# Kernel optimization log

Measured on AMD Instinct MI355X. Metric: run time of the kernel, lower is better.

The kernel has to match this reference:

```python
import jax, jax.numpy as jnp
import numpy as np

N_VERTICES = 1_000_000
N_EDGES = 16_000_000


def setup_inputs() -> dict:
    key = jax.random.key(0)
    k1, k2, k3 = jax.random.split(key, 3)
    vertex_attr = jax.random.normal(k1, (N_VERTICES, 2), dtype=jnp.float32)
    edgeij_pair = jax.random.randint(k2, (2, N_EDGES), 0, N_VERTICES, dtype=jnp.int64)
    edge_attr = jax.random.normal(k3, (N_EDGES, 2), dtype=jnp.float32)
    g = jnp.zeros((1, 1), dtype=jnp.float32)
    batch = jnp.zeros((N_VERTICES,), dtype=jnp.int64)
    return {"vertex_attr": vertex_attr, "edgeij_pair": edgeij_pair,
            "edge_attr": edge_attr, "g": g, "batch": batch}


def reference(vertex_attr, edgeij_pair, edge_attr, g, batch):
    # c_ij: second edge feature column, [E, 1]
    c_ij = edge_attr[:, 1:2]
    b_i = vertex_attr[:, 0:1]  # [N, 1]
    x_i = vertex_attr[:, 1:2]  # [N, 1]
    n_vertices = x_i.shape[0]
    # edge-to-vertex aggregation: sum c_ij into receiving vertex i (row 0)
    cbar_i = jax.ops.segment_sum(c_ij, edgeij_pair[0], num_segments=n_vertices)
    r_i = b_i - cbar_i
    return jnp.concatenate([b_i, x_i, r_i], axis=1)  # [N, 3]
```

## Files before the change

kernel.cpp:

```cpp
#include <hip/hip_runtime.h>


#define BSHIFT 11
#define BSIZE (1 << BSHIFT)
#define NBUCK_PAD 512
#define TILE 8192
#define TPB 1024
#define PGRID 512
#define NREP 8

#define BARL() do { \
    asm volatile("s_waitcnt lgkmcnt(0)" ::: "memory"); \
    __builtin_amdgcn_s_barrier(); } while (0)

__global__ __launch_bounds__(TPB, 8)
void vu_partition(const int* __restrict__ src,
                  const float* __restrict__ eattr,
                  unsigned long long* __restrict__ pairs,
                  unsigned int* __restrict__ alloc,
                  int ne, int nbuck, int cap_r) {
    __shared__ unsigned long long sorted[TILE];
    __shared__ unsigned int hist[NBUCK_PAD];
    __shared__ unsigned int base_l[NBUCK_PAD];
    __shared__ unsigned int cursor[NBUCK_PAD];
    __shared__ unsigned int gbase[NBUCK_PAD];
    __shared__ unsigned int wsum[8];

    const int t = threadIdx.x;
    const int rep = blockIdx.x & (NREP - 1);
    const int nt_tiles = (ne + TILE - 1) / TILE;

    int   s0, s1, s2, s3, s4, s5, s6, s7;
    float c0, c1, c2, c3, c4, c5, c6, c7;

    int tk = blockIdx.x;

    if (tk < nt_tiles) {
        int tile0 = tk * TILE;
        if (tile0 + TILE <= ne) {
            const int* sp = src + tile0 + t;
            const float* cp = eattr + 2 * (tile0 + t) + 1;
            s0 = sp[0 * 1024]; s1 = sp[1 * 1024];
            s2 = sp[2 * 1024]; s3 = sp[3 * 1024];
            s4 = sp[4 * 1024]; s5 = sp[5 * 1024];
            s6 = sp[6 * 1024]; s7 = sp[7 * 1024];
            c0 = cp[0 * 2048]; c1 = cp[1 * 2048];
            c2 = cp[2 * 2048]; c3 = cp[3 * 2048];
            c4 = cp[4 * 2048]; c5 = cp[5 * 2048];
            c6 = cp[6 * 2048]; c7 = cp[7 * 2048];
        }
    }
    if (t < NBUCK_PAD) hist[t] = 0u;
    BARL();

    for (; tk < nt_tiles; tk += PGRID) {
        int tile0 = tk * TILE;
        int lim = ne - tile0; if (lim > TILE) lim = TILE;
        bool full = (lim == TILE);

        int nk = tk + PGRID;
        bool pv = (nk < nt_tiles) && (nk * TILE + TILE <= ne);
        int   p0s, p1s, p2s, p3s, p4s, p5s, p6s, p7s;
        float p0c, p1c, p2c, p3c, p4c, p5c, p6c, p7c;
        if (pv) {
            int ptile0 = nk * TILE;
            const int* sp = src + ptile0 + t;
            const float* cp = eattr + 2 * (ptile0 + t) + 1;
            p0s = sp[0 * 1024]; p1s = sp[1 * 1024];
            p2s = sp[2 * 1024]; p3s = sp[3 * 1024];
            p4s = sp[4 * 1024]; p5s = sp[5 * 1024];
            p6s = sp[6 * 1024]; p7s = sp[7 * 1024];
            p0c = cp[0 * 2048]; p1c = cp[1 * 2048];
            p2c = cp[2 * 2048]; p3c = cp[3 * 2048];
            p4c = cp[4 * 2048]; p5c = cp[5 * 2048];
            p6c = cp[6 * 2048]; p7c = cp[7 * 2048];
        }

        if (full) {
            atomicAdd(&hist[((unsigned)s0) >> BSHIFT], 1u);
            atomicAdd(&hist[((unsigned)s1) >> BSHIFT], 1u);
            atomicAdd(&hist[((unsigned)s2) >> BSHIFT], 1u);
            atomicAdd(&hist[((unsigned)s3) >> BSHIFT], 1u);
            atomicAdd(&hist[((unsigned)s4) >> BSHIFT], 1u);
            atomicAdd(&hist[((unsigned)s5) >> BSHIFT], 1u);
            atomicAdd(&hist[((unsigned)s6) >> BSHIFT], 1u);
            atomicAdd(&hist[((unsigned)s7) >> BSHIFT], 1u);
        } else {
            for (int i = t; i < lim; i += TPB)
                atomicAdd(&hist[((unsigned)src[tile0 + i]) >> BSHIFT], 1u);
        }
        BARL();

        unsigned int mycnt = (t < NBUCK_PAD) ? hist[t] : 0u;
        if (t < NBUCK_PAD) hist[t] = 0u;
        unsigned int gb = 0u;
        if (t < nbuck && mycnt)
            gb = atomicAdd(&alloc[rep * NBUCK_PAD + t], mycnt);

        unsigned int x = mycnt;
        #pragma unroll
        for (int off = 1; off < 64; off <<= 1) {
            unsigned int v = __shfl_up(x, off, 64);
            if ((t & 63) >= off) x += v;
        }
        if (t < NBUCK_PAD && (t & 63) == 63) wsum[t >> 6] = x;
        BARL();

        unsigned int wx = 0u;
        int wid = t >> 6;
        #pragma unroll
        for (int k = 0; k < 7; ++k) {
            unsigned int w = wsum[k];
            if (k < wid) wx += w;
        }
        if (t < NBUCK_PAD) {
            unsigned int excl = x + wx - mycnt;
            base_l[t] = excl;
            cursor[t] = excl;
            gbase[t] = gb;
        }
        BARL();

#define VU_SCAT(sv, cv) do { \
        unsigned int q_ = ((unsigned)(sv)) >> BSHIFT; \
        unsigned int pos_ = atomicAdd(&cursor[q_], 1u); \
        sorted[pos_] = ((unsigned long long)__float_as_uint(cv) << 32) \
                       | (unsigned)(sv); } while (0)
        if (full) {
            VU_SCAT(s0, c0); VU_SCAT(s1, c1);
            VU_SCAT(s2, c2); VU_SCAT(s3, c3);
            VU_SCAT(s4, c4); VU_SCAT(s5, c5);
            VU_SCAT(s6, c6); VU_SCAT(s7, c7);
        } else {
            for (int i = t; i < lim; i += TPB) {
                int e = tile0 + i;
                int s = src[e];
                float2 ec = ((const float2*)eattr)[e];
                VU_SCAT(s, ec.y);
            }
        }
#undef VU_SCAT
        BARL();

        for (int i = t; i < lim; i += TPB) {
            unsigned long long p = sorted[i];
            unsigned int q = ((unsigned int)p) >> BSHIFT;
            unsigned int seg = (q << 3) + (unsigned int)rep;
            unsigned int dst = seg * (unsigned int)cap_r + gbase[q]
                             + ((unsigned int)i - base_l[q]);
            unsigned int hi = seg * (unsigned int)cap_r + (unsigned int)cap_r - 1u;
            if (dst > hi) dst = hi;
            pairs[dst] = p;
        }

        s0 = p0s; s1 = p1s; s2 = p2s; s3 = p3s;
        s4 = p4s; s5 = p5s; s6 = p6s; s7 = p7s;
        c0 = p0c; c1 = p1c; c2 = p2c; c3 = p3c;
        c4 = p4c; c5 = p5c; c6 = p6c; c7 = p7c;
    }
}

__global__ __launch_bounds__(1024)
void vu_aggregate(const unsigned long long* __restrict__ pairs,
                  const unsigned int* __restrict__ alloc,
                  const float* __restrict__ vattr,
                  float* __restrict__ out,
                  int nv, int cap_r) {
    __shared__ float acc[BSIZE];
    __shared__ float obuf[BSIZE * 3];
    int q = blockIdx.x;
    int t = threadIdx.x;
    acc[t] = 0.0f;
    acc[t + 1024] = 0.0f;

    int v0 = q << BSHIFT;
    int iv0 = v0 + t, iv1 = v0 + t + 1024;
    float2 va0 = make_float2(0.f, 0.f), va1 = make_float2(0.f, 0.f);
    if (iv0 < nv) va0 = ((const float2*)vattr)[iv0];
    if (iv1 < nv) va1 = ((const float2*)vattr)[iv1];

    unsigned int cnts[NREP];
    #pragma unroll
    for (int r = 0; r < NREP; ++r) {
        unsigned int c = alloc[r * NBUCK_PAD + q];
        cnts[r] = (c > (unsigned int)cap_r) ? (unsigned int)cap_r : c;
    }
    __syncthreads();

#define VU_ACC(v64) do { \
        atomicAdd(&acc[((unsigned int)(v64)) & (BSIZE - 1)], \
                  __uint_as_float((unsigned int)((v64) >> 32))); } while (0)

    #pragma unroll
    for (int r = 0; r < NREP; ++r) {
        unsigned int cnt = cnts[r];
        const unsigned long long* p =
            pairs + (size_t)(q * NREP + r) * (size_t)cap_r;
        const ulonglong2* p2 = (const ulonglong2*)p;
        unsigned int n2 = cnt >> 1;
        for (unsigned int i = t; i < n2; i += 1024u) {
            ulonglong2 v = p2[i];
            VU_ACC(v.x); VU_ACC(v.y);
        }
        if (t == 0 && (cnt & 1u)) {
            unsigned long long v = p[cnt - 1];
            VU_ACC(v);
        }
    }
#undef VU_ACC
    __syncthreads();

    if (iv0 < nv) {
        obuf[3 * t + 0] = va0.x;
        obuf[3 * t + 1] = va0.y;
        obuf[3 * t + 2] = va0.x - acc[t];
    }
    {
        int i2 = t + 1024;
        if (iv1 < nv) {
            obuf[3 * i2 + 0] = va1.x;
            obuf[3 * i2 + 1] = va1.y;
            obuf[3 * i2 + 2] = va1.x - acc[i2];
        }
    }
    __syncthreads();

    long fbase = (long)q * (BSIZE * 3);
    int nfl = 3 * nv - (int)fbase;
    if (nfl > BSIZE * 3) nfl = BSIZE * 3;
    if (nfl > 0) {
        float4* o4 = (float4*)(out + fbase);
        const float4* s4 = (const float4*)obuf;
        int n4 = nfl >> 2;
        for (int j = t; j < n4; j += 1024) o4[j] = s4[j];
        for (int j = (n4 << 2) + t; j < nfl; j += 1024) out[fbase + j] = obuf[j];
    }
}

__global__ void vu_init_kernel(const float* __restrict__ vattr,
                               float* __restrict__ out, int n) {
    int i = blockIdx.x * blockDim.x + threadIdx.x;
    if (i < n) {
        float2 v = ((const float2*)vattr)[i];
        out[3 * i + 0] = v.x;
        out[3 * i + 1] = v.y;
        out[3 * i + 2] = v.x;
    }
}

__global__ void vu_scatter_kernel(const int* __restrict__ src,
                                  const float* __restrict__ eattr,
                                  float* __restrict__ out, int ne) {
    int t = blockIdx.x * blockDim.x + threadIdx.x;
    int e0 = t * 4;
    if (e0 + 3 < ne) {
        int4 idx = ((const int4*)src)[t];
        float4 a = ((const float4*)eattr)[2 * t + 0];
        float4 b = ((const float4*)eattr)[2 * t + 1];
        atomicAdd(&out[3 * idx.x + 2], -a.y);
        atomicAdd(&out[3 * idx.y + 2], -a.w);
        atomicAdd(&out[3 * idx.z + 2], -b.y);
        atomicAdd(&out[3 * idx.w + 2], -b.w);
    } else {
        for (int e = e0; e < ne; ++e)
            atomicAdd(&out[3 * src[e] + 2], -eattr[2 * e + 1]);
    }
}

extern "C" void kernel_launch(void* const* d_in, const int* in_sizes, int n_in,
                              void* d_out, int out_size, void* d_ws, size_t ws_size,
                              hipStream_t stream) {
    const float* vattr = (const float*)d_in[0];
    const int* edges = (const int*)d_in[1];
    const float* eattr = (const float*)d_in[2];
    float* out = (float*)d_out;

    int nv = in_sizes[0] / 2;
    int ne = in_sizes[2] / 2;

    int nbuck = (nv + BSIZE - 1) >> BSHIFT;
    int mean_r = ne / nbuck / NREP;
    int cap_r = mean_r + mean_r / 8;
    cap_r = (cap_r + 15) & ~15;

    size_t alloc_bytes = (size_t)NREP * NBUCK_PAD * 4;
    size_t pair_bytes = (size_t)nbuck * NREP * (size_t)cap_r * 8ull;
    size_t need = alloc_bytes + pair_bytes;

    if (ws_size >= need && nbuck <= NBUCK_PAD) {
        unsigned int* alloc = (unsigned int*)d_ws;
        unsigned long long* pairs = (unsigned long long*)((char*)d_ws + alloc_bytes);
        (void)hipMemsetAsync(alloc, 0, alloc_bytes, stream);

        int nt_tiles = (ne + TILE - 1) / TILE;
        int grid = PGRID; if (grid > nt_tiles) grid = nt_tiles;
        vu_partition<<<grid, TPB, 0, stream>>>(edges, eattr, pairs, alloc,
                                               ne, nbuck, cap_r);
        vu_aggregate<<<nbuck, 1024, 0, stream>>>(pairs, alloc, vattr, out,
                                                 nv, cap_r);
    } else {
        int threads = 256;
        int blocks = (nv + threads - 1) / threads;
        vu_init_kernel<<<blocks, threads, 0, stream>>>(vattr, out, nv);
        int nt = (ne + 3) / 4;
        blocks = (nt + threads - 1) / threads;
        vu_scatter_kernel<<<blocks, threads, 0, stream>>>(edges, eattr, out, ne);
    }
}
```

Baseline: 373.3 us.

## Replace persistent prefetching partition loop with one-tile-per-block launch and vector loads

The partition kernel no longer runs as a persistent grid that loops over tiles with software prefetch of the next tile. It now launches one 512-thread block per 4096-edge tile, loading each thread's 8 consecutive sources and edge attributes with int4/float4 vector loads. The hist array is reused to hold the global bases, dropping the separate gbase array and cutting shared memory so more blocks can be resident. This trades the register-level prefetch overlap for occupancy-driven latency hiding, at the cost of more blocks and more global atomics on alloc. Each block's output runs are also shorter.

```diff
diff --git a/kernel.cpp b/kernel.cpp
--- a/kernel.cpp
+++ b/kernel.cpp
@@ -4,9 +4,8 @@
 #define BSHIFT 11
 #define BSIZE (1 << BSHIFT)
 #define NBUCK_PAD 512
-#define TILE 8192
-#define TPB 1024
-#define PGRID 512
+#define TILE 4096
+#define TPB 512
 #define NREP 8
 
 #define BARL() do { \
@@ -23,140 +22,98 @@
     __shared__ unsigned int hist[NBUCK_PAD];
     __shared__ unsigned int base_l[NBUCK_PAD];
     __shared__ unsigned int cursor[NBUCK_PAD];
-    __shared__ unsigned int gbase[NBUCK_PAD];
     __shared__ unsigned int wsum[8];
 
     const int t = threadIdx.x;
     const int rep = blockIdx.x & (NREP - 1);
-    const int nt_tiles = (ne + TILE - 1) / TILE;
-
-    int   s0, s1, s2, s3, s4, s5, s6, s7;
+    const int tile0 = blockIdx.x * TILE;
+    int lim = ne - tile0; if (lim > TILE) lim = TILE;
+    const bool full = (lim == TILE);
+
+    hist[t] = 0u;
+    BARL();
+
+    int4 sa, sb;
     float c0, c1, c2, c3, c4, c5, c6, c7;
-
-    int tk = blockIdx.x;
-
-    if (tk < nt_tiles) {
-        int tile0 = tk * TILE;
-        if (tile0 + TILE <= ne) {
-            const int* sp = src + tile0 + t;
-            const float* cp = eattr + 2 * (tile0 + t) + 1;
-            s0 = sp[0 * 1024]; s1 = sp[1 * 1024];
-            s2 = sp[2 * 1024]; s3 = sp[3 * 1024];
-            s4 = sp[4 * 1024]; s5 = sp[5 * 1024];
-            s6 = sp[6 * 1024]; s7 = sp[7 * 1024];
-            c0 = cp[0 * 2048]; c1 = cp[1 * 2048];
-            c2 = cp[2 * 2048]; c3 = cp[3 * 2048];
-            c4 = cp[4 * 2048]; c5 = cp[5 * 2048];
-            c6 = cp[6 * 2048]; c7 = cp[7 * 2048];
-        }
-    }
-    if (t < NBUCK_PAD) hist[t] = 0u;
-    BARL();
-
-    for (; tk < nt_tiles; tk += PGRID) {
-        int tile0 = tk * TILE;
-        int lim = ne - tile0; if (lim > TILE) lim = TILE;
-        bool full = (lim == TILE);
-
-        int nk = tk + PGRID;
-        bool pv = (nk < nt_tiles) && (nk * TILE + TILE <= ne);
-        int   p0s, p1s, p2s, p3s, p4s, p5s, p6s, p7s;
-        float p0c, p1c, p2c, p3c, p4c, p5c, p6c, p7c;
-        if (pv) {
-            int ptile0 = nk * TILE;
-            const int* sp = src + ptile0 + t;
-            const float* cp = eattr + 2 * (ptile0 + t) + 1;
-            p0s = sp[0 * 1024]; p1s = sp[1 * 1024];
-            p2s = sp[2 * 1024]; p3s = sp[3 * 1024];
-            p4s = sp[4 * 1024]; p5s = sp[5 * 1024];
-            p6s = sp[6 * 1024]; p7s = sp[7 * 1024];
-            p0c = cp[0 * 2048]; p1c = cp[1 * 2048];
-            p2c = cp[2 * 2048]; p3c = cp[3 * 2048];
-            p4c = cp[4 * 2048]; p5c = cp[5 * 2048];
-            p6c = cp[6 * 2048]; p7c = cp[7 * 2048];
-        }
-
-        if (full) {
-            atomicAdd(&hist[((unsigned)s0) >> BSHIFT], 1u);
-            atomicAdd(&hist[((unsigned)s1) >> BSHIFT], 1u);
-            atomicAdd(&hist[((unsigned)s2) >> BSHIFT], 1u);
-            atomicAdd(&hist[((unsigned)s3) >> BSHIFT], 1u);
-            atomicAdd(&hist[((unsigned)s4) >> BSHIFT], 1u);
-            atomicAdd(&hist[((unsigned)s5) >> BSHIFT], 1u);
-            atomicAdd(&hist[((unsigned)s6) >> BSHIFT], 1u);
-            atomicAdd(&hist[((unsigned)s7) >> BSHIFT], 1u);
-        } else {
-            for (int i = t; i < lim; i += TPB)
-                atomicAdd(&hist[((unsigned)src[tile0 + i]) >> BSHIFT], 1u);
-        }
-        BARL();
-
-        unsigned int mycnt = (t < NBUCK_PAD) ? hist[t] : 0u;
-        if (t < NBUCK_PAD) hist[t] = 0u;
-        unsigned int gb = 0u;
-        if (t < nbuck && mycnt)
-            gb = atomicAdd(&alloc[rep * NBUCK_PAD + t], mycnt);
-
-        unsigned int x = mycnt;
-        #pragma unroll
-        for (int off = 1; off < 64; off <<= 1) {
-            unsigned int v = __shfl_up(x, off, 64);
-            if ((t & 63) >= off) x += v;
-        }
-        if (t < NBUCK_PAD && (t & 63) == 63) wsum[t >> 6] = x;
-        BARL();
-
-        unsigned int wx = 0u;
-        int wid = t >> 6;
-        #pragma unroll
-        for (int k = 0; k < 7; ++k) {
-            unsigned int w = wsum[k];
-            if (k < wid) wx += w;
-        }
-        if (t < NBUCK_PAD) {
-            unsigned int excl = x + wx - mycnt;
-            base_l[t] = excl;
-            cursor[t] = excl;
-            gbase[t] = gb;
-        }
-        BARL();
+    if (full) {
+        const int4* s4 = (const int4*)(src + tile0) + 2 * t;
+        sa = s4[0];
+        sb = s4[1];
+        const float4* e4 = (const float4*)(eattr + 2 * (size_t)tile0) + 4 * t;
+        float4 e0 = e4[0], e1 = e4[1], e2 = e4[2], e3 = e4[3];
+        c0 = e0.y; c1 = e0.w; c2 = e1.y; c3 = e1.w;
+        c4 = e2.y; c5 = e2.w; c6 = e3.y; c7 = e3.w;
+        atomicAdd(&hist[((unsigned)sa.x) >> BSHIFT], 1u);
+        atomicAdd(&hist[((unsigned)sa.y) >> BSHIFT], 1u);
+        atomicAdd(&hist[((unsigned)sa.z) >> BSHIFT], 1u);
+        atomicAdd(&hist[((unsigned)sa.w) >> BSHIFT], 1u);
+        atomicAdd(&hist[((unsigned)sb.x) >> BSHIFT], 1u);
+        atomicAdd(&hist[((unsigned)sb.y) >> BSHIFT], 1u);
+        atomicAdd(&hist[((unsigned)sb.z) >> BSHIFT], 1u);
+        atomicAdd(&hist[((unsigned)sb.w) >> BSHIFT], 1u);
+    } else {
+        for (int i = t; i < lim; i += TPB)
+            atomicAdd(&hist[((unsigned)src[tile0 + i]) >> BSHIFT], 1u);
+    }
+    BARL();
+
+    unsigned int mycnt = hist[t];
+    unsigned int gb = 0u;
+    if (t < nbuck && mycnt)
+        gb = atomicAdd(&alloc[rep * NBUCK_PAD + t], mycnt);
+
+    unsigned int x = mycnt;
+    #pragma unroll
+    for (int off = 1; off < 64; off <<= 1) {
+        unsigned int v = __shfl_up(x, off, 64);
+        if ((t & 63) >= off) x += v;
+    }
+    if ((t & 63) == 63) wsum[t >> 6] = x;
+    BARL();
+
+    unsigned int wx = 0u;
+    int wid = t >> 6;
+    #pragma unroll
+    for (int k = 0; k < 7; ++k) {
+        unsigned int w = wsum[k];
+        if (k < wid) wx += w;
+    }
+    unsigned int excl = x + wx - mycnt;
+    base_l[t] = excl;
+    cursor[t] = excl;
+    hist[t] = gb;
+    BARL();
 
 #define VU_SCAT(sv, cv) do { \
         unsigned int q_ = ((unsigned)(sv)) >> BSHIFT; \
         unsigned int pos_ = atomicAdd(&cursor[q_], 1u); \
         sorted[pos_] = ((unsigned long long)__float_as_uint(cv) << 32) \
                        | (unsigned)(sv); } while (0)
-        if (full) {
-            VU_SCAT(s0, c0); VU_SCAT(s1, c1);
-            VU_SCAT(s2, c2); VU_SCAT(s3, c3);
-            VU_SCAT(s4, c4); VU_SCAT(s5, c5);
-            VU_SCAT(s6, c6); VU_SCAT(s7, c7);
-        } else {
-            for (int i = t; i < lim; i += TPB) {
-                int e = tile0 + i;
-                int s = src[e];
-                float2 ec = ((const float2*)eattr)[e];
-                VU_SCAT(s, ec.y);
-            }
-        }
+    if (full) {
+        VU_SCAT(sa.x, c0); VU_SCAT(sa.y, c1);
+        VU_SCAT(sa.z, c2); VU_SCAT(sa.w, c3);
+        VU_SCAT(sb.x, c4); VU_SCAT(sb.y, c5);
+        VU_SCAT(sb.z, c6); VU_SCAT(sb.w, c7);
+    } else {
+        for (int i = t; i < lim; i += TPB) {
+            int e = tile0 + i;
+            int s = src[e];
+            float2 ec = ((const float2*)eattr)[e];
+            VU_SCAT(s, ec.y);
+        }
+    }
 #undef VU_SCAT
-        BARL();
-
-        for (int i = t; i < lim; i += TPB) {
-            unsigned long long p = sorted[i];
-            unsigned int q = ((unsigned int)p) >> BSHIFT;
-            unsigned int seg = (q << 3) + (unsigned int)rep;
-            unsigned int dst = seg * (unsigned int)cap_r + gbase[q]
-                             + ((unsigned int)i - base_l[q]);
-            unsigned int hi = seg * (unsigned int)cap_r + (unsigned int)cap_r - 1u;
-            if (dst > hi) dst = hi;
-            pairs[dst] = p;
-        }
-
-        s0 = p0s; s1 = p1s; s2 = p2s; s3 = p3s;
-        s4 = p4s; s5 = p5s; s6 = p6s; s7 = p7s;
-        c0 = p0c; c1 = p1c; c2 = p2c; c3 = p3c;
-        c4 = p4c; c5 = p5c; c6 = p6c; c7 = p7c;
+    BARL();
+
+    for (int i = t; i < lim; i += TPB) {
+        unsigned long long p = sorted[i];
+        unsigned int q = ((unsigned int)p) >> BSHIFT;
+        unsigned int seg = (q << 3) + (unsigned int)rep;
+        unsigned int dst = seg * (unsigned int)cap_r + hist[q]
+                         + ((unsigned int)i - base_l[q]);
+        unsigned int hi = seg * (unsigned int)cap_r + (unsigned int)cap_r - 1u;
+        if (dst > hi) dst = hi;
+        pairs[dst] = p;
     }
 }
 
@@ -293,9 +250,8 @@
         (void)hipMemsetAsync(alloc, 0, alloc_bytes, stream);
 
         int nt_tiles = (ne + TILE - 1) / TILE;
-        int grid = PGRID; if (grid > nt_tiles) grid = nt_tiles;
-        vu_partition<<<grid, TPB, 0, stream>>>(edges, eattr, pairs, alloc,
-                                               ne, nbuck, cap_r);
+        vu_partition<<<nt_tiles, TPB, 0, stream>>>(edges, eattr, pairs, alloc,
+                                                   ne, nbuck, cap_r);
         vu_aggregate<<<nbuck, 1024, 0, stream>>>(pairs, alloc, vattr, out,
                                                  nv, cap_r);
     } else {
```

After: 366.9 us. Within noise of the previous version (-1.7%).
